# Kernel optimization log

Measured on AMD Instinct MI355X. Metric: run time of the kernel, lower is better.

## Reference

```python
import jax, jax.numpy as jnp
from jax import lax
import numpy as np

# dims
VOCAB = 64
B, L = 64, 2048
EMB = 128
D_MODEL = 128
N_LAYERS = 4
D_INNER = 256      # expand=2
D_STATE = 16
D_CONV = 4
DT_RANK = 8        # ceil(d_model/16)
NCLS = 3
BN_EPS = 1e-5
RMS_EPS = 1e-5


def setup_inputs():
    key = jax.random.key(0)
    ks = iter(jax.random.split(key, 48))
    def rn(shape, s=0.02):
        return jax.random.normal(next(ks), shape, jnp.float32) * s
    tokens = jax.random.randint(next(ks), (B, L), 0, VOCAB)
    mask = jnp.ones((B, L), jnp.float32)
    emb = rn((VOCAB, EMB)).at[0].set(0.0)  # padding_idx=0
    bn_w = jnp.ones((EMB,), jnp.float32)
    bn_b = jnp.zeros((EMB,), jnp.float32)
    conv_w = rn((D_MODEL, EMB, 3))
    conv_b = jnp.zeros((D_MODEL,), jnp.float32)
    in_proj_w = rn((N_LAYERS, 2 * D_INNER, D_MODEL))
    conv1d_w = rn((N_LAYERS, D_INNER, D_CONV), 0.1)
    conv1d_b = jnp.zeros((N_LAYERS, D_INNER), jnp.float32)
    x_proj_w = rn((N_LAYERS, DT_RANK + 2 * D_STATE, D_INNER))
    dt_proj_w = rn((N_LAYERS, D_INNER, DT_RANK), 0.1)
    dt_proj_b = rn((N_LAYERS, D_INNER), 0.1)
    A_log = jnp.tile(jnp.log(jnp.arange(1, D_STATE + 1, dtype=jnp.float32))[None, None, :],
                     (N_LAYERS, D_INNER, 1))
    D_param = jnp.ones((N_LAYERS, D_INNER), jnp.float32)
    out_proj_w = rn((N_LAYERS, D_MODEL, D_INNER))
    norm_w = jnp.ones((N_LAYERS, D_MODEL), jnp.float32)
    lin1_w = rn((512, D_MODEL)); lin1_b = jnp.zeros((512,), jnp.float32)
    lin2_w = rn((512, 512));     lin2_b = jnp.zeros((512,), jnp.float32)
    lin3_w = rn((NCLS, 512));    lin3_b = jnp.zeros((NCLS,), jnp.float32)
    return dict(tokens=tokens, mask=mask, emb=emb, bn_w=bn_w, bn_b=bn_b,
                conv_w=conv_w, conv_b=conv_b, in_proj_w=in_proj_w,
                conv1d_w=conv1d_w, conv1d_b=conv1d_b, x_proj_w=x_proj_w,
                dt_proj_w=dt_proj_w, dt_proj_b=dt_proj_b, A_log=A_log,
                D_param=D_param, out_proj_w=out_proj_w, norm_w=norm_w,
                lin1_w=lin1_w, lin1_b=lin1_b, lin2_w=lin2_w, lin2_b=lin2_b,
                lin3_w=lin3_w, lin3_b=lin3_b)


def _rmsnorm(x, w):
    return x * lax.rsqrt(jnp.mean(x * x, axis=-1, keepdims=True) + RMS_EPS) * w


def _selective_scan(u, dt, A, Bm, Cm, Dv):
    # u, dt: (B,L,di); A: (di,ds); Bm, Cm: (B,L,ds); Dv: (di,)
    def step(h, inp):
        dt_t, B_t, C_t, u_t = inp           # (B,di),(B,ds),(B,ds),(B,di)
        dA = jnp.exp(dt_t[:, :, None] * A)  # (B,di,ds)
        h = dA * h + (dt_t * u_t)[:, :, None] * B_t[:, None, :]
        y = jnp.einsum('bds,bs->bd', h, C_t)
        return h, y
    h0 = jnp.zeros((u.shape[0], A.shape[0], A.shape[1]), u.dtype)
    xs = (jnp.swapaxes(dt, 0, 1), jnp.swapaxes(Bm, 0, 1),
          jnp.swapaxes(Cm, 0, 1), jnp.swapaxes(u, 0, 1))
    _, ys = lax.scan(step, h0, xs)          # ys: (L,B,di)
    return jnp.swapaxes(ys, 0, 1) + u * Dv


def _mamba(x, in_w, cw, cb, xp_w, dtp_w, dtp_b, A_log, Dv, out_w):
    # x: (B,L,d_model)
    xz = jnp.einsum('bld,ed->ble', x, in_w)            # (B,L,2*di)
    xi, z = jnp.split(xz, 2, axis=-1)
    # causal depthwise conv over time
    xc = jnp.swapaxes(xi, 1, 2)                        # (B,di,L)
    xc = lax.conv_general_dilated(xc, cw[:, None, :], (1,), [(D_CONV - 1, 0)],
                                  dimension_numbers=('NCH', 'OIH', 'NCH'),
                                  feature_group_count=D_INNER)
    xc = jax.nn.silu(xc + cb[None, :, None])
    xc = jnp.swapaxes(xc, 1, 2)                        # (B,L,di)
    x_dbl = jnp.einsum('bld,ed->ble', xc, xp_w)        # (B,L,dtr+2*ds)
    dt = jax.nn.softplus(jnp.einsum('blr,dr->bld', x_dbl[..., :DT_RANK], dtp_w) + dtp_b)
    Bm = x_dbl[..., DT_RANK:DT_RANK + D_STATE]
    Cm = x_dbl[..., DT_RANK + D_STATE:]
    A = -jnp.exp(A_log)                                # (di,ds)
    y = _selective_scan(xc, dt, A, Bm, Cm, Dv)
    y = y * jax.nn.silu(z)
    return jnp.einsum('ble,de->bld', y, out_w)         # (B,L,d_model)


def _forward(tokens, mask, emb, bn_w, bn_b, conv_w, conv_b, in_proj_w,
             conv1d_w, conv1d_b, x_proj_w, dt_proj_w, dt_proj_b, A_log,
             D_param, out_proj_w, norm_w, lin1_w, lin1_b, lin2_w, lin2_b,
             lin3_w, lin3_b):
    x = emb[tokens]                                    # (B,L,E)
    xc = jnp.swapaxes(x, 1, 2)                         # (B,E,L)
    # BatchNorm1d in eval mode: running_mean=0, running_var=1
    xc = xc * (bn_w * lax.rsqrt(jnp.array(1.0 + BN_EPS)))[None, :, None] + bn_b[None, :, None]
    xc = lax.conv_general_dilated(xc, conv_w, (1,), [(1, 1)],
                                  dimension_numbers=('NCH', 'OIH', 'NCH'))
    xc = jax.nn.relu(xc + conv_b[None, :, None])
    x = jnp.swapaxes(xc, 1, 2)                         # (B,L,D_MODEL)
    for i in range(N_LAYERS):
        x = _mamba(_rmsnorm(x, norm_w[i]), in_proj_w[i], conv1d_w[i],
                   conv1d_b[i], x_proj_w[i], dt_proj_w[i], dt_proj_b[i],
                   A_log[i], D_param[i], out_proj_w[i]) + x
    # masked average pooling
    m = mask[:, :, None]
    denom = jnp.clip(jnp.sum(m, axis=1), 1e-9, None)   # (B,1)->(B,D) broadcast
    pooled = jnp.sum(x * m, axis=1) / denom
    h = jax.nn.relu(pooled @ lin1_w.T + lin1_b)
    h = jax.nn.relu(h @ lin2_w.T + lin2_b)
    return h @ lin3_w.T + lin3_b                       # (B,NCLS)


def reference(tokens, mask, emb, bn_w, bn_b, conv_w, conv_b, in_proj_w,
              conv1d_w, conv1d_b, x_proj_w, dt_proj_w, dt_proj_b, A_log,
              D_param, out_proj_w, norm_w, lin1_w, lin1_b, lin2_w, lin2_b,
              lin3_w, lin3_b):
    return _forward(tokens, mask, emb, bn_w, bn_b, conv_w, conv_b, in_proj_w,
                    conv1d_w, conv1d_b, x_proj_w, dt_proj_w, dt_proj_b, A_log,
                    D_param, out_proj_w, norm_w, lin1_w, lin1_b, lin2_w,
                    lin2_b, lin3_w, lin3_b)
```

## Files before the change

kernel.cpp:

```cpp
#include <hip/hip_runtime.h>
#include <math.h>

#define NB     64
#define SL     2048
#define NTOK   (NB*SL)
#define EMB_D  128
#define DMODEL 128
#define DIN    256
#define DST    16
#define NLAYER 4
#define SEG    64
#define NSEG   (SL/SEG)
#define L2E    1.4426950408889634f
#define LN2    0.6931471805599453f

typedef __bf16 bf16x8 __attribute__((ext_vector_type(8)));
typedef __bf16 bf16x4 __attribute__((ext_vector_type(4)));
typedef float  f32x4  __attribute__((ext_vector_type(4)));
typedef float  f32x2  __attribute__((ext_vector_type(2)));

#define FIX_PL   ((size_t)0)
#define FIX_PM   (FIX_PL + 131072)
#define FIX_PD   (FIX_PM + 1024)
#define FIX_H1   (FIX_PD + 8192)
#define FIX_H2   (FIX_H1 + 32768)
#define FIX_WP   (FIX_H2 + 32768)
#define FIX_W2B  (FIX_WP + 65536)
#define FIX_WINB (FIX_W2B + 24576)
#define FIX_WOUTB (FIX_WINB + 131072)
#define FIX_END  (FIX_WOUTB + 65536)

__device__ __forceinline__ float fexp2(float x){ return __builtin_amdgcn_exp2f(x); }
__device__ __forceinline__ float flog2(float x){ return __builtin_amdgcn_logf(x); }
__device__ __forceinline__ float frcp (float x){ return __builtin_amdgcn_rcpf(x); }
__device__ __forceinline__ float fast_exp(float x){ return fexp2(x*L2E); }
__device__ __forceinline__ float siluf(float v){ return v * frcp(1.f + fast_exp(-v)); }
__device__ __forceinline__ float softplusf(float a){
  return fmaxf(a,0.f) + flog2(1.f + fexp2(-fabsf(a)*L2E)) * LN2;
}
__device__ __forceinline__ unsigned short bfbits(float x){
  __bf16 b = (__bf16)x; return __builtin_bit_cast(unsigned short, b);
}
__device__ __forceinline__ unsigned int packdu(float dt, float u){
  return ((unsigned int)bfbits(u) << 16) | (unsigned int)bfbits(dt);
}

__device__ __forceinline__ f32x2 pkfma(f32x2 a, f32x2 b, f32x2 c){
#if __has_builtin(__builtin_elementwise_fma)
  return __builtin_elementwise_fma(a, b, c);
#else
  return (f32x2){ fmaf(a.x,b.x,c.x), fmaf(a.y,b.y,c.y) };
#endif
}

__global__ void k_w2b(const float* __restrict__ cw, __bf16* __restrict__ w2){
  int g = blockIdx.x*256 + threadIdx.x;
  if (g >= 128*384) return;
  int d = g / 384, j = g % 384;
  int k = j >> 7, e = j & 127;
  w2[d*384 + k*128 + e] = (__bf16)cw[d*384 + e*3 + k];
}

__global__ void k_cvt(const float* __restrict__ src, __bf16* __restrict__ dst, int n){
  int i = blockIdx.x*256 + threadIdx.x;
  if (i < n) dst[i] = (__bf16)src[i];
}

__global__ void k_wprep(const float* __restrict__ xpw, __bf16* __restrict__ wp){
  int g = blockIdx.x*256 + threadIdx.x;
  int l = g >> 14, rem = g & 16383;
  int n = rem >> 8, k = rem & 255;
  float v = (n < 40) ? xpw[(size_t)l*40*256 + n*256 + k] : 0.f;
  wp[g] = (__bf16)v;
}

__global__ void k_embed(const int* __restrict__ tok, const float* __restrict__ emb,
                        const float* __restrict__ bnw, const float* __restrict__ bnb,
                        float* __restrict__ xp){
  int r = blockIdx.x;
  int e = threadIdx.x;
  int b = r / 2050, tp = r % 2050;
  float v = 0.f;
  if (tp != 0 && tp != 2049){
    int t = tp - 1;
    int id = tok[(size_t)b*SL + t];
    float s = bnw[e] * rsqrtf(1.0f + 1e-5f);
    v = emb[(size_t)id*EMB_D + e] * s + bnb[e];
  }
  xp[(size_t)r*EMB_D + e] = v;
}

__global__ __launch_bounds__(256) void k_rmsscale(const float* __restrict__ x,
                                                  float* __restrict__ rs){
  int wv = threadIdx.x>>6, lane = threadIdx.x&63;
  size_t tok = (size_t)blockIdx.x*4 + wv;
  float2 v = *(const float2*)(x + tok*128 + lane*2);
  float ss = v.x*v.x + v.y*v.y;
  #pragma unroll
  for (int m=1;m<64;m<<=1) ss += __shfl_xor(ss, m);
  float r = rsqrtf(ss*(1.f/128.f) + 1e-5f);
  if (lane == 0) rs[tok] = r;
}

template<int MODE, int K, int N>
__global__ __launch_bounds__(256) void k_mgemm(
    const void* __restrict__ Av, const __bf16* __restrict__ Wb,
    const float* __restrict__ bias, const float* __restrict__ rsp,
    const float* __restrict__ nwp,
    float* __restrict__ out, __bf16* __restrict__ outb, __bf16* __restrict__ outz){
  __shared__ __bf16 As[128][40];
  __shared__ __bf16 Bs[128][40];
  const int tid  = threadIdx.x;
  const int wave = tid >> 6;
  const int lane = tid & 63;
  const int col  = lane & 15;
  const int quad = lane >> 4;
  const int wm = (wave & 1) * 64;
  const int wn = (wave >> 1) * 64;
  const int m0 = blockIdx.y * 128;
  const int n0 = blockIdx.x * 128;

  f32x4 acc[4][4];
  #pragma unroll
  for (int i=0;i<4;i++)
    #pragma unroll
    for (int j=0;j<4;j++) acc[i][j] = (f32x4){0.f,0.f,0.f,0.f};

  size_t abase;
  if constexpr(MODE==0){
    int bb = m0 >> 11, tloc = m0 & 2047;
    abase = ((size_t)bb*2050 + tloc) * 128;
  } else {
    abase = (size_t)m0 * K;
  }

  const int sm = tid >> 3;
  const int sk4 = (tid & 7) * 4;
  const int bn = tid >> 2;
  const int bk8 = (tid & 3) * 8;

  for (int k0 = 0; k0 < K; k0 += 32){
    #pragma unroll
    for (int p=0;p<4;p++){
      int m = p*32 + sm;
      const float* A = (const float*)Av;
      float4 v;
      if constexpr(MODE==0){
        v = *(const float4*)(A + abase + (size_t)m*128 + k0 + sk4);
      } else {
        float4 x4 = *(const float4*)(A + abase + (size_t)m*K + k0 + sk4);
        float4 w4 = *(const float4*)(nwp + k0 + sk4);
        float s = rsp[m0 + m];
        v.x = x4.x*s*w4.x; v.y = x4.y*s*w4.y; v.z = x4.z*s*w4.z; v.w = x4.w*s*w4.w;
      }
      bf16x4 o;
      o[0] = (__bf16)v.x; o[1] = (__bf16)v.y; o[2] = (__bf16)v.z; o[3] = (__bf16)v.w;
      *(bf16x4*)&As[m][sk4] = o;
    }
    #pragma unroll
    for (int p=0;p<2;p++){
      int n = p*64 + bn;
      bf16x8 w = *(const bf16x8*)(Wb + (size_t)(n0+n)*K + k0 + bk8);
      *(bf16x8*)&Bs[n][bk8] = w;
    }
    __syncthreads();
    bf16x8 af[4], bfr[4];
    const int fq = quad*8;
    #pragma unroll
    for (int i=0;i<4;i++) af[i]  = *(const bf16x8*)&As[wm + i*16 + col][fq];
    #pragma unroll
    for (int j=0;j<4;j++) bfr[j] = *(const bf16x8*)&Bs[wn + j*16 + col][fq];
    #pragma unroll
    for (int i=0;i<4;i++)
      #pragma unroll
      for (int j=0;j<4;j++)
        acc[i][j] = __builtin_amdgcn_mfma_f32_16x16x32_bf16(af[i], bfr[j], acc[i][j], 0, 0, 0);
    __syncthreads();
  }

  #pragma unroll
  for (int i=0;i<4;i++){
    #pragma unroll
    for (int j=0;j<4;j++){
      int n_l = wn + j*16 + col;
      #pragma unroll
      for (int r=0;r<4;r++){
        int m = m0 + wm + i*16 + quad*4 + r;
        float c = acc[i][j][r];
        if constexpr(MODE==0){
          int n = n0 + n_l;
          out[(size_t)m*DMODEL + n] = fmaxf(c + bias[n], 0.f);
        } else {
          int n = n0 + n_l;
          if (n < DIN) outb[(size_t)m*DIN + n]        = (__bf16)c;
          else         outz[(size_t)m*DIN + n - DIN]  = (__bf16)siluf(c);
        }
      }
    }
  }
}

__global__ __launch_bounds__(256) void k_seg(const __bf16* __restrict__ xi,
    const __bf16* __restrict__ wpb,
    const float* __restrict__ cw, const float* __restrict__ cb,
    const float* __restrict__ dtw, const float* __restrict__ dtb,
    const float* __restrict__ alog,
    float* __restrict__ vbc, unsigned int* __restrict__ dub,
    float* __restrict__ cseg, float* __restrict__ sdtb){
  __shared__ __bf16 sxc[64][264];
  __shared__ float vls[64][68];
  const int tid = threadIdx.x;
  const size_t m0 = (size_t)blockIdx.x * 64;
  const int b = (int)(m0 >> 11);
  const int g = (int)((m0 >> 6) & (NSEG-1));
  const int seq0 = (int)(m0 & 2047);

  {
    const int c4 = (tid & 63) * 4;
    const int tw = tid >> 6;
    float wc[4][4];
    #pragma unroll
    for (int j=0;j<4;j++)
      #pragma unroll
      for (int k=0;k<4;k++) wc[j][k] = cw[(c4+j)*4 + k];
    float4 cb4 = *(const float4*)(cb + c4);
    #pragma unroll
    for (int it=0; it<16; it++){
      int t = it*4 + tw;
      float4 acc = cb4;
      #pragma unroll
      for (int k=0;k<4;k++){
        if (seq0 + t - 3 + k >= 0){
          bf16x4 xv = *(const bf16x4*)(xi + (m0 + t - 3 + k)*DIN + c4);
          acc.x = fmaf(wc[0][k], (float)xv[0], acc.x);
          acc.y = fmaf(wc[1][k], (float)xv[1], acc.y);
          acc.z = fmaf(wc[2][k], (float)xv[2], acc.z);
          acc.w = fmaf(wc[3][k], (float)xv[3], acc.w);
        }
      }
      bf16x4 o;
      o[0]=(__bf16)siluf(acc.x); o[1]=(__bf16)siluf(acc.y);
      o[2]=(__bf16)siluf(acc.z); o[3]=(__bf16)siluf(acc.w);
      *(bf16x4*)&sxc[t][c4] = o;
    }
  }
  __syncthreads();

  {
    const int wave = tid >> 6, lane = tid & 63;
    const int col = lane & 15, quad = lane >> 4;
    const int wn = wave * 16;
    f32x4 acc[4];
    #pragma unroll
    for (int i=0;i<4;i++) acc[i] = (f32x4){0.f,0.f,0.f,0.f};
    #pragma unroll
    for (int kc=0;kc<8;kc++){
      bf16x8 bfr = *(const bf16x8*)(wpb + (size_t)(wn+col)*256 + kc*32 + quad*8);
      #pragma unroll
      for (int mi=0;mi<4;mi++){
        bf16x8 af = *(const bf16x8*)&sxc[mi*16 + col][kc*32 + quad*8];
        acc[mi] = __builtin_amdgcn_mfma_f32_16x16x32_bf16(af, bfr, acc[mi], 0, 0, 0);
      }
    }
    #pragma unroll
    for (int mi=0;mi<4;mi++)
      #pragma unroll
      for (int r=0;r<4;r++)
        vls[mi*16 + quad*4 + r][wn + col] = acc[mi][r];
  }
  __syncthreads();

  #pragma unroll
  for (int p=0;p<8;p++){
    int j = p*256 + tid;
    int t = j >> 5, i = j & 31;
    vbc[(m0+t)*32 + i] = vls[t][8+i];
  }

  {
    const int d = tid;
    const float a0 = -fast_exp(alog[d*DST]) * L2E;
    bool fast = true;
    for (int s=1;s<16;s++){
      float as = -fast_exp(alog[d*DST + s]) * L2E;
      fast = fast && (fabsf(as - (float)(s+1)*a0) <= 1e-3f*fabsf(as));
    }
    float4 w8a = *(const float4*)(dtw + d*8);
    float4 w8b = *(const float4*)(dtw + d*8 + 4);
    const f32x2 wA0 = {w8a.x, w8a.y}, wA1 = {w8a.z, w8a.w};
    const f32x2 wB0 = {w8b.x, w8b.y}, wB1 = {w8b.z, w8b.w};
    const float bd = dtb[d];
    float ssum = 0.f;
    size_t base = (((size_t)b*NSEG + g)*DIN + d)*DST;
    if (fast){
      f32x2 hp[8];
      #pragma unroll
      for (int k=0;k<8;k++) hp[k] = (f32x2){0.f,0.f};
      for (int t=0;t<SEG;t++){
        float4 v0 = *(const float4*)&vls[t][0];
        float4 v1 = *(const float4*)&vls[t][4];
        f32x2 la = pkfma((f32x2){v0.x,v0.y}, wA0, (f32x2){bd, 0.f});
        la = pkfma((f32x2){v0.z,v0.w}, wA1, la);
        la = pkfma((f32x2){v1.x,v1.y}, wB0, la);
        la = pkfma((f32x2){v1.z,v1.w}, wB1, la);
        float dt = softplusf(la.x + la.y);
        ssum += dt;
        float u = (float)sxc[t][d];
        dub[(m0+t)*DIN + d] = packdu(dt, u);
        float du = dt*u;
        float r1 = fexp2(dt*a0);
        float r2 = r1*r1, r4 = r2*r2, r8 = r4*r4;
        f32x2 p01 = {r1, r2};
        f32x2 s2 = {r2, r2}, s4 = {r4, r4}, s8 = {r8, r8};
        f32x2 p23 = p01*s2, p45 = p01*s4, p67 = p23*s4;
        f32x2 p89 = p01*s8, pAB = p23*s8, pCD = p45*s8, pEF = p67*s8;
        float4 b0 = *(const float4*)&vls[t][8];
        float4 b1 = *(const float4*)&vls[t][12];
        float4 b2 = *(const float4*)&vls[t][16];
        float4 b3 = *(const float4*)&vls[t][20];
        f32x2 du2 = {du, du};
        hp[0] = pkfma(p01, hp[0], du2*(f32x2){b0.x,b0.y});
        hp[1] = pkfma(p23, hp[1], du2*(f32x2){b0.z,b0.w});
        hp[2] = pkfma(p45, hp[2], du2*(f32x2){b1.x,b1.y});
        hp[3] = pkfma(p67, hp[3], du2*(f32x2){b1.z,b1.w});
        hp[4] = pkfma(p89, hp[4], du2*(f32x2){b2.x,b2.y});
        hp[5] = pkfma(pAB, hp[5], du2*(f32x2){b2.z,b2.w});
        hp[6] = pkfma(pCD, hp[6], du2*(f32x2){b3.x,b3.y});
        hp[7] = pkfma(pEF, hp[7], du2*(f32x2){b3.z,b3.w});
      }
      #pragma unroll
      for (int k=0;k<4;k++){
        float4 o = { hp[2*k].x, hp[2*k].y, hp[2*k+1].x, hp[2*k+1].y };
        *(float4*)(cseg + base + 4*k) = o;
      }
    } else {
      float h[16];
      float aA[16];
      #pragma unroll
      for (int k=0;k<16;k++){ h[k] = 0.f; aA[k] = -fast_exp(alog[d*DST + k]) * L2E; }
      for (int t=0;t<SEG;t++){
        float4 v0 = *(const float4*)&vls[t][0];
        float4 v1 = *(const float4*)&vls[t][4];
        float lin = bd;
        lin = fmaf(v0.x,w8a.x, fmaf(v0.y,w8a.y, fmaf(v0.z,w8a.z, fmaf(v0.w,w8a.w, lin))));
        lin = fmaf(v1.x,w8b.x, fmaf(v1.y,w8b.y, fmaf(v1.z,w8b.z, fmaf(v1.w,w8b.w, lin))));
        float dt = softplusf(lin);
        ssum += dt;
        float u = (float)sxc[t][d];
        dub[(m0+t)*DIN + d] = packdu(dt, u);
        float du = dt*u;
        #pragma unroll
        for (int k=0;k<16;k++){
          float e = fexp2(dt*aA[k]);
          h[k] = fmaf(e, h[k], du*vls[t][8+k]);
        }
      }
      #pragma unroll
      for (int k=0;k<4;k++){
        float4 o = { h[4*k], h[4*k+1], h[4*k+2], h[4*k+3] };
        *(float4*)(cseg + base + 4*k) = o;
      }
    }
    sdtb[((size_t)b*NSEG + g)*DIN + d] = ssum;
  }
}

__global__ __launch_bounds__(256) void k_scanB(float* __restrict__ cseg,
    const float* __restrict__ sdtb, const float* __restrict__ alog){
  int gl = blockIdx.x*256 + threadIdx.x;
  int b   = gl >> 12;
  int rem = gl & 4095;
  int d = rem >> 4, s = rem & 15;
  const float a = -fast_exp(alog[d*DST + s]) * L2E;
  float h = 0.f;
  for (int g=0; g<NSEG; g++){
    size_t base = ((size_t)b*NSEG + g)*DIN;
    float sd = sdtb[base + d];
    size_t ci = (base + d)*DST + s;
    float c = cseg[ci];
    cseg[ci] = h;
    h = fmaf(fexp2(a*sd), h, c);
  }
}

__global__ __launch_bounds__(256) void k_scanC3(float* __restrict__ xres,
    const unsigned int* __restrict__ dub, const float* __restrict__ vbc,
    const __bf16* __restrict__ gzb,
    const float* __restrict__ alog, const float* __restrict__ Dpar,
    const float* __restrict__ cseg, const __bf16* __restrict__ wout,
    float* __restrict__ rs){
  __shared__ __bf16 sy[64][264];
  __shared__ float svbc[64][32];
  float* sx = (float*)sy;
  const int tid = threadIdx.x;
  const size_t m0 = (size_t)blockIdx.x * 64;
  const int b = (int)(m0 >> 11);
  const int g = (int)((m0 >> 6) & (NSEG-1));

  #pragma unroll
  for (int p=0;p<8;p++){
    int j = p*256 + tid;
    int t = j >> 5, i = j & 31;
    svbc[t][i] = vbc[(m0+t)*32 + i];
  }

  {
    const int d = tid;
    const float a0 = -fast_exp(alog[d*DST]) * L2E;
    bool fast = true;
    for (int s=1;s<16;s++){
      float as = -fast_exp(alog[d*DST + s]) * L2E;
      fast = fast && (fabsf(as - (float)(s+1)*a0) <= 1e-3f*fabsf(as));
    }
    const float Dv = Dpar[d];
    size_t base = (((size_t)b*NSEG + g)*DIN + d)*DST;
    float4 hv0 = *(const float4*)(cseg + base);
    float4 hv1 = *(const float4*)(cseg + base + 4);
    float4 hv2 = *(const float4*)(cseg + base + 8);
    float4 hv3 = *(const float4*)(cseg + base + 12);
    __syncthreads();

    if (fast){
      f32x2 hp[8] = { {hv0.x,hv0.y},{hv0.z,hv0.w},{hv1.x,hv1.y},{hv1.z,hv1.w},
                      {hv2.x,hv2.y},{hv2.z,hv2.w},{hv3.x,hv3.y},{hv3.z,hv3.w} };

#define LOADCH(WV,GV,T0) \
      _Pragma("unroll") \
      for (int q=0;q<8;q++){ \
        WV[q] = dub[(m0 + (T0) + q)*DIN + d]; \
        GV[q] = gzb[(m0 + (T0) + q)*DIN + d]; \
      }

#define SCSTEP(T,WW,GG) { \
      float u  = __builtin_bit_cast(float, (WW) & 0xffff0000u); \
      float dt = __builtin_bit_cast(float, (WW) << 16); \
      float du = dt*u; \
      float r1 = fexp2(dt*a0); \
      float r2 = r1*r1, r4 = r2*r2, r8 = r4*r4; \
      f32x2 p01 = {r1, r2}; \
      f32x2 s2 = {r2, r2}, s4 = {r4, r4}, s8 = {r8, r8}; \
      f32x2 p23 = p01*s2, p45 = p01*s4, p67 = p23*s4; \
      f32x2 p89 = p01*s8, pAB = p23*s8, pCD = p45*s8, pEF = p67*s8; \
      float4 b0 = *(const float4*)&svbc[T][0]; \
      float4 b1 = *(const float4*)&svbc[T][4]; \
      float4 b2 = *(const float4*)&svbc[T][8]; \
      float4 b3 = *(const float4*)&svbc[T][12]; \
      float4 c0 = *(const float4*)&svbc[T][16]; \
      float4 c1 = *(const float4*)&svbc[T][20]; \
      float4 c2 = *(const float4*)&svbc[T][24]; \
      float4 c3 = *(const float4*)&svbc[T][28]; \
      f32x2 du2 = {du, du}; \
      f32x2 ya = {0.f,0.f}, yb = {0.f,0.f}; \
      hp[0] = pkfma(p01, hp[0], du2*(f32x2){b0.x,b0.y}); \
      ya = pkfma(hp[0], (f32x2){c0.x,c0.y}, ya); \
      hp[1] = pkfma(p23, hp[1], du2*(f32x2){b0.z,b0.w}); \
      yb = pkfma(hp[1], (f32x2){c0.z,c0.w}, yb); \
      hp[2] = pkfma(p45, hp[2], du2*(f32x2){b1.x,b1.y}); \
      ya = pkfma(hp[2], (f32x2){c1.x,c1.y}, ya); \
      hp[3] = pkfma(p67, hp[3], du2*(f32x2){b1.z,b1.w}); \
      yb = pkfma(hp[3], (f32x2){c1.z,c1.w}, yb); \
      hp[4] = pkfma(p89, hp[4], du2*(f32x2){b2.x,b2.y}); \
      ya = pkfma(hp[4], (f32x2){c2.x,c2.y}, ya); \
      hp[5] = pkfma(pAB, hp[5], du2*(f32x2){b2.z,b2.w}); \
      yb = pkfma(hp[5], (f32x2){c2.z,c2.w}, yb); \
      hp[6] = pkfma(pCD, hp[6], du2*(f32x2){b3.x,b3.y}); \
      ya = pkfma(hp[6], (f32x2){c3.x,c3.y}, ya); \
      hp[7] = pkfma(pEF, hp[7], du2*(f32x2){b3.z,b3.w}); \
      yb = pkfma(hp[7], (f32x2){c3.z,c3.w}, yb); \
      f32x2 ys = ya + yb; \
      float y = ys.x + ys.y; \
      sy[T][d] = (__bf16)((y + u*Dv) * (float)(GG)); }

      unsigned int wv0[8], wv1[8];
      __bf16 gv0[8], gv1[8];
      LOADCH(wv0, gv0, 0)
      #pragma unroll
      for (int tc=0; tc<SEG; tc+=16){
        LOADCH(wv1, gv1, tc+8)
        #pragma unroll
        for (int q=0;q<8;q++){ SCSTEP(tc+q, wv0[q], gv0[q]) }
        if (tc+16 < SEG){ LOADCH(wv0, gv0, tc+16) }
        #pragma unroll
        for (int q=0;q<8;q++){ SCSTEP(tc+8+q, wv1[q], gv1[q]) }
      }
#undef LOADCH
#undef SCSTEP
    } else {
      float h[16] = {hv0.x,hv0.y,hv0.z,hv0.w, hv1.x,hv1.y,hv1.z,hv1.w,
                     hv2.x,hv2.y,hv2.z,hv2.w, hv3.x,hv3.y,hv3.z,hv3.w};
      float aA[16];
      #pragma unroll
      for (int k=0;k<16;k++) aA[k] = -fast_exp(alog[d*DST + k]) * L2E;
      for (int t=0;t<SEG;t++){
        unsigned int w = dub[(m0+t)*DIN + d];
        float u  = __builtin_bit_cast(float, w & 0xffff0000u);
        float dt = __builtin_bit_cast(float, w << 16);
        float du = dt*u;
        float y = 0.f;
        #pragma unroll
        for (int k=0;k<16;k++){
          float e = fexp2(dt*aA[k]);
          h[k] = fmaf(e, h[k], du*svbc[t][k]);
          y = fmaf(h[k], svbc[t][16+k], y);
        }
        float gz = (float)gzb[(m0+t)*DIN + d];
        sy[t][d] = (__bf16)((y + u*Dv) * gz);
      }
    }
  }
  __syncthreads();

  const int wave = tid >> 6, lane = tid & 63;
  const int col = lane & 15, quad = lane >> 4;
  const int wn = wave * 32;
  f32x4 acc[4][2];
  #pragma unroll
  for (int i=0;i<4;i++)
    #pragma unroll
    for (int j=0;j<2;j++) acc[i][j] = (f32x4){0.f,0.f,0.f,0.f};
  #pragma unroll
  for (int kc=0;kc<8;kc++){
    bf16x8 bfr0 = *(const bf16x8*)(wout + (size_t)(wn +      col)*256 + kc*32 + quad*8);
    bf16x8 bfr1 = *(const bf16x8*)(wout + (size_t)(wn + 16 + col)*256 + kc*32 + quad*8);
    #pragma unroll
    for (int mi=0;mi<4;mi++){
      bf16x8 af = *(const bf16x8*)&sy[mi*16 + col][kc*32 + quad*8];
      acc[mi][0] = __builtin_amdgcn_mfma_f32_16x16x32_bf16(af, bfr0, acc[mi][0], 0, 0, 0);
      acc[mi][1] = __builtin_amdgcn_mfma_f32_16x16x32_bf16(af, bfr1, acc[mi][1], 0, 0, 0);
    }
  }
  __syncthreads();

  #pragma unroll
  for (int mi=0;mi<4;mi++){
    #pragma unroll
    for (int j=0;j<2;j++){
      int n = wn + j*16 + col;
      #pragma unroll
      for (int r=0;r<4;r++){
        int ml = mi*16 + quad*4 + r;
        size_t go = (m0 + ml)*DMODEL + n;
        float nx = xres[go] + acc[mi][j][r];
        xres[go] = nx;
        sx[ml*132 + n] = nx;
      }
    }
  }
  __syncthreads();
  {
    int row = tid >> 2, q = tid & 3;
    const float* pr = sx + row*132 + q*32;
    float ss = 0.f;
    #pragma unroll
    for (int i=0;i<32;i+=4){
      float4 v = *(const float4*)(pr + i);
      ss += v.x*v.x + v.y*v.y + v.z*v.z + v.w*v.w;
    }
    ss += __shfl_xor(ss, 1);
    ss += __shfl_xor(ss, 2);
    if (q == 0) rs[m0 + row] = rsqrtf(ss*(1.f/128.f) + 1e-5f);
  }
}

__global__ __launch_bounds__(256) void k_pool1(const float* __restrict__ x,
    const float* __restrict__ mask, float* __restrict__ part, float* __restrict__ pmask){
  int b = blockIdx.y, seg = blockIdx.x;
  int d = threadIdx.x & 127, half = threadIdx.x >> 7;
  int t0 = seg*128 + half*64;
  float acc = 0.f, macc = 0.f;
  for (int i=0;i<64;i++){
    int t = t0 + i;
    float mv = mask[(size_t)b*SL + t];
    acc = fmaf(x[((size_t)b*SL + t)*DMODEL + d], mv, acc);
    macc += mv;
  }
  __shared__ float sm[256];
  __shared__ float smm[2];
  sm[threadIdx.x] = acc;
  if (d == 0) smm[half] = macc;
  __syncthreads();
  if (half == 0){
    part[((size_t)b*16 + seg)*128 + d] = sm[d] + sm[128+d];
    if (d == 0) pmask[b*16 + seg] = smm[0] + smm[1];
  }
}

__global__ void k_pool2(const float* __restrict__ part, const float* __restrict__ pmask,
                        float* __restrict__ pooled){
  int b = blockIdx.x, d = threadIdx.x;
  float acc = 0.f, ms = 0.f;
  for (int s=0;s<16;s++){ acc += part[((size_t)b*16+s)*128 + d]; ms += pmask[b*16+s]; }
  pooled[(size_t)b*128 + d] = acc / fmaxf(ms, 1e-9f);
}

__global__ void k_mlp_a(const float* __restrict__ in, const float* __restrict__ w,
                        const float* __restrict__ bias, float* __restrict__ out, int K){
  int b = blockIdx.y;
  int n = blockIdx.x*128 + threadIdx.x;
  const float4* pw = (const float4*)(w + (size_t)n*K);
  const float4* pi = (const float4*)(in + (size_t)b*K);
  float acc = 0.f;
  for (int k=0;k<K/4;k++){
    float4 a = pi[k], ww = pw[k];
    acc = fmaf(a.x,ww.x, fmaf(a.y,ww.y, fmaf(a.z,ww.z, fmaf(a.w,ww.w, acc))));
  }
  out[(size_t)b*512 + n] = fmaxf(acc + bias[n], 0.f);
}

__global__ void k_mlp3(const float* __restrict__ h, const float* __restrict__ w,
                       const float* __restrict__ bias, float* __restrict__ out){
  int b = blockIdx.x;
  int n = threadIdx.x >> 6, lane = threadIdx.x & 63;
  if (n >= 3) return;
  float acc = 0.f;
  for (int k=lane; k<512; k+=64) acc = fmaf(h[(size_t)b*512+k], w[(size_t)n*512+k], acc);
  #pragma unroll
  for (int m=1;m<64;m<<=1) acc += __shfl_xor(acc, m);
  if (lane == 0) out[(size_t)b*3 + n] = acc + bias[n];
}

extern "C" void kernel_launch(void* const* d_in, const int* in_sizes, int n_in,
                              void* d_out, int out_size, void* d_ws, size_t ws_size,
                              hipStream_t stream){
  const int*   tokens = (const int*)  d_in[0];
  const float* mask   = (const float*)d_in[1];
  const float* emb    = (const float*)d_in[2];
  const float* bn_w   = (const float*)d_in[3];
  const float* bn_b   = (const float*)d_in[4];
  const float* conv_w = (const float*)d_in[5];
  const float* conv_b = (const float*)d_in[6];
  const float* in_w   = (const float*)d_in[7];
  const float* c1_w   = (const float*)d_in[8];
  const float* c1_b   = (const float*)d_in[9];
  const float* xp_w   = (const float*)d_in[10];
  const float* dtp_w  = (const float*)d_in[11];
  const float* dtp_b  = (const float*)d_in[12];
  const float* A_log  = (const float*)d_in[13];
  const float* D_par  = (const float*)d_in[14];
  const float* out_w  = (const float*)d_in[15];
  const float* nrm_w  = (const float*)d_in[16];
  const float* l1w = (const float*)d_in[17]; const float* l1b = (const float*)d_in[18];
  const float* l2w = (const float*)d_in[19]; const float* l2b = (const float*)d_in[20];
  const float* l3w = (const float*)d_in[21]; const float* l3b = (const float*)d_in[22];
  float* dout = (float*)d_out;

  int CB = 64;
  while (CB > 1 && ((size_t)CB*SL*741 + FIX_END)*4 > ws_size) CB >>= 1;
  if (((size_t)CB*SL*741 + FIX_END)*4 > ws_size) return;
  const size_t CTOK = (size_t)CB*SL;

  float* ws  = (float*)d_ws;
  float* pl  = ws + FIX_PL;
  float* pm  = ws + FIX_PM;
  float* pd  = ws + FIX_PD;
  float* h1  = ws + FIX_H1;
  float* h2  = ws + FIX_H2;
  __bf16* wpb   = (__bf16*)(ws + FIX_WP);
  __bf16* w2b   = (__bf16*)(ws + FIX_W2B);
  __bf16* winb  = (__bf16*)(ws + FIX_WINB);
  __bf16* woutb = (__bf16*)(ws + FIX_WOUTB);
  float* xcb = ws + FIX_END;
  float* rs  = xcb + CTOK*128;
  __bf16* xib = (__bf16*)(rs + CTOK);
  unsigned int* dub = (unsigned int*)(xib + CTOK*256);
  float* pad = (float*)xib;
  float* vbc = (float*)(dub + CTOK*256);
  float* csg = vbc + CTOK*32;
  float* sdt = csg + CTOK*64;
  __bf16* zb  = (__bf16*)(sdt + CTOK*4);

  k_w2b<<<192, 256, 0, stream>>>(conv_w, w2b);
  k_cvt<<<1024, 256, 0, stream>>>(in_w,  winb,  4*512*128);
  k_cvt<<<512,  256, 0, stream>>>(out_w, woutb, 4*128*256);
  k_wprep<<<256, 256, 0, stream>>>(xp_w, wpb);

  const int nchunks = NB / CB;
  for (int c = 0; c < nchunks; c++){
    const int* tok_c = tokens + (size_t)c*CTOK;

    k_embed<<<CB*2050, 128, 0, stream>>>(tok_c, emb, bn_w, bn_b, pad);
    k_mgemm<0,384,128><<<dim3(1, CTOK/128), 256, 0, stream>>>(
        pad, w2b, conv_b, nullptr, nullptr, xcb, nullptr, nullptr);
    k_rmsscale<<<CTOK/4, 256, 0, stream>>>(xcb, rs);

    for (int layer = 0; layer < NLAYER; layer++){
      const __bf16* lin = winb  + (size_t)layer*512*128;
      const float* lcw  = c1_w  + (size_t)layer*DIN*4;
      const float* lcb  = c1_b  + (size_t)layer*DIN;
      const float* ldw  = dtp_w + (size_t)layer*DIN*8;
      const float* ldb  = dtp_b + (size_t)layer*DIN;
      const float* lal  = A_log + (size_t)layer*DIN*DST;
      const float* lD   = D_par + (size_t)layer*DIN;
      const __bf16* low = woutb + (size_t)layer*128*256;
      const float* lnw  = nrm_w + (size_t)layer*128;

      k_mgemm<1,128,512><<<dim3(4, CTOK/128), 256, 0, stream>>>(
          xcb, lin, nullptr, rs, lnw, nullptr, xib, zb);
      k_seg<<<(int)(CTOK/64), 256, 0, stream>>>(
          xib, wpb + (size_t)layer*64*256, lcw, lcb, ldw, ldb, lal, vbc, dub, csg, sdt);
      k_scanB<<<CB*16, 256, 0, stream>>>(csg, sdt, lal);
      k_scanC3<<<(int)(CTOK/64), 256, 0, stream>>>(
          xcb, dub, vbc, zb, lal, lD, csg, low, rs);
    }

    k_pool1<<<dim3(16, CB), 256, 0, stream>>>(
        xcb, mask + (size_t)c*CTOK, pl + (size_t)c*CB*16*128, pm + (size_t)c*CB*16);
  }

  k_pool2<<<NB, 128, 0, stream>>>(pl, pm, pd);
  k_mlp_a<<<dim3(4, NB), 128, 0, stream>>>(pd, l1w, l1b, h1, 128);
  k_mlp_a<<<dim3(4, NB), 128, 0, stream>>>(h1, l2w, l2b, h2, 512);
  k_mlp3<<<NB, 256, 0, stream>>>(h2, l3w, l3b, dout);
}
```

Before: 1.389 ms.

## Fuse embedding into conv GEMM, fuse MLP head, prefetch scan operands

Embedding lookup and batchnorm scaling now happen inside the first GEMM's A-tile load, so the padded embedding buffer is never written and read back. The pooling and three MLP layers become one kernel per batch row. The depthwise conv in k_seg keeps a sliding register window instead of reloading four rows per output. The k_seg and scanC loops load next-step LDS operands one iteration ahead, and scanB loads all segment values before its serial recurrence. These changes remove launches and memory traffic and hide latency, at the cost of more registers, which can lower occupancy.

```diff
diff --git a/kernel.cpp b/kernel.cpp
--- a/kernel.cpp
+++ b/kernel.cpp
@@ -74,22 +74,6 @@
   wp[g] = (__bf16)v;
 }
 
-__global__ void k_embed(const int* __restrict__ tok, const float* __restrict__ emb,
-                        const float* __restrict__ bnw, const float* __restrict__ bnb,
-                        float* __restrict__ xp){
-  int r = blockIdx.x;
-  int e = threadIdx.x;
-  int b = r / 2050, tp = r % 2050;
-  float v = 0.f;
-  if (tp != 0 && tp != 2049){
-    int t = tp - 1;
-    int id = tok[(size_t)b*SL + t];
-    float s = bnw[e] * rsqrtf(1.0f + 1e-5f);
-    v = emb[(size_t)id*EMB_D + e] * s + bnb[e];
-  }
-  xp[(size_t)r*EMB_D + e] = v;
-}
-
 __global__ __launch_bounds__(256) void k_rmsscale(const float* __restrict__ x,
                                                   float* __restrict__ rs){
   int wv = threadIdx.x>>6, lane = threadIdx.x&63;
@@ -106,7 +90,7 @@
 __global__ __launch_bounds__(256) void k_mgemm(
     const void* __restrict__ Av, const __bf16* __restrict__ Wb,
     const float* __restrict__ bias, const float* __restrict__ rsp,
-    const float* __restrict__ nwp,
+    const float* __restrict__ nwp, const float* __restrict__ bnbp,
     float* __restrict__ out, __bf16* __restrict__ outb, __bf16* __restrict__ outz){
   __shared__ __bf16 As[128][40];
   __shared__ __bf16 Bs[128][40];
@@ -126,36 +110,54 @@
     #pragma unroll
     for (int j=0;j<4;j++) acc[i][j] = (f32x4){0.f,0.f,0.f,0.f};
 
-  size_t abase;
-  if constexpr(MODE==0){
-    int bb = m0 >> 11, tloc = m0 & 2047;
-    abase = ((size_t)bb*2050 + tloc) * 128;
-  } else {
-    abase = (size_t)m0 * K;
-  }
-
   const int sm = tid >> 3;
   const int sk4 = (tid & 7) * 4;
   const int bn = tid >> 2;
   const int bk8 = (tid & 3) * 8;
 
   for (int k0 = 0; k0 < K; k0 += 32){
-    #pragma unroll
-    for (int p=0;p<4;p++){
-      int m = p*32 + sm;
-      const float* A = (const float*)Av;
-      float4 v;
-      if constexpr(MODE==0){
-        v = *(const float4*)(A + abase + (size_t)m*128 + k0 + sk4);
-      } else {
+    if constexpr(MODE==0){
+      const int* tok = (const int*)Av;
+      const int tap = k0 >> 7;
+      const int e = (k0 & 127) + sk4;
+      const float sc = rsqrtf(1.0f + 1e-5f);
+      float4 bw4 = *(const float4*)(nwp + e);
+      float4 bb4 = *(const float4*)(bnbp + e);
+      float4 s4;
+      s4.x = bw4.x*sc; s4.y = bw4.y*sc; s4.z = bw4.z*sc; s4.w = bw4.w*sc;
+      #pragma unroll
+      for (int p=0;p<4;p++){
+        int m = p*32 + sm;
+        int tokpos = m0 + m;
+        int t = (tokpos & 2047) + tap - 1;
+        float4 v = {0.f,0.f,0.f,0.f};
+        if ((unsigned)t < 2048u){
+          int id = tok[((size_t)(tokpos >> 11) << 11) + t];
+          float4 ev = *(const float4*)(rsp + (size_t)id*EMB_D + e);
+          v.x = fmaf(ev.x, s4.x, bb4.x);
+          v.y = fmaf(ev.y, s4.y, bb4.y);
+          v.z = fmaf(ev.z, s4.z, bb4.z);
+          v.w = fmaf(ev.w, s4.w, bb4.w);
+        }
+        bf16x4 o;
+        o[0] = (__bf16)v.x; o[1] = (__bf16)v.y; o[2] = (__bf16)v.z; o[3] = (__bf16)v.w;
+        *(bf16x4*)&As[m][sk4] = o;
+      }
+    } else {
+      const size_t abase = (size_t)m0 * K;
+      #pragma unroll
+      for (int p=0;p<4;p++){
+        int m = p*32 + sm;
+        const float* A = (const float*)Av;
         float4 x4 = *(const float4*)(A + abase + (size_t)m*K + k0 + sk4);
         float4 w4 = *(const float4*)(nwp + k0 + sk4);
         float s = rsp[m0 + m];
+        float4 v;
         v.x = x4.x*s*w4.x; v.y = x4.y*s*w4.y; v.z = x4.z*s*w4.z; v.w = x4.w*s*w4.w;
-      }
-      bf16x4 o;
-      o[0] = (__bf16)v.x; o[1] = (__bf16)v.y; o[2] = (__bf16)v.z; o[3] = (__bf16)v.w;
-      *(bf16x4*)&As[m][sk4] = o;
+        bf16x4 o;
+        o[0] = (__bf16)v.x; o[1] = (__bf16)v.y; o[2] = (__bf16)v.z; o[3] = (__bf16)v.w;
+        *(bf16x4*)&As[m][sk4] = o;
+      }
     }
     #pragma unroll
     for (int p=0;p<2;p++){
@@ -218,30 +220,42 @@
   {
     const int c4 = (tid & 63) * 4;
     const int tw = tid >> 6;
+    const int t0 = tw * 16;
     float wc[4][4];
     #pragma unroll
     for (int j=0;j<4;j++)
       #pragma unroll
       for (int k=0;k<4;k++) wc[j][k] = cw[(c4+j)*4 + k];
     float4 cb4 = *(const float4*)(cb + c4);
-    #pragma unroll
-    for (int it=0; it<16; it++){
-      int t = it*4 + tw;
+    bf16x4 zed;
+    zed[0] = (__bf16)0.f; zed[1] = (__bf16)0.f; zed[2] = (__bf16)0.f; zed[3] = (__bf16)0.f;
+    bf16x4 win[3];
+    #pragma unroll
+    for (int j=0;j<3;j++){
+      int tr = t0 - 3 + j;
+      win[j] = (seq0 + tr >= 0) ? *(const bf16x4*)(xi + (m0 + tr)*DIN + c4) : zed;
+    }
+    #pragma unroll
+    for (int i=0;i<16;i++){
+      int t = t0 + i;
+      bf16x4 w3 = *(const bf16x4*)(xi + (m0 + t)*DIN + c4);
       float4 acc = cb4;
       #pragma unroll
-      for (int k=0;k<4;k++){
-        if (seq0 + t - 3 + k >= 0){
-          bf16x4 xv = *(const bf16x4*)(xi + (m0 + t - 3 + k)*DIN + c4);
-          acc.x = fmaf(wc[0][k], (float)xv[0], acc.x);
-          acc.y = fmaf(wc[1][k], (float)xv[1], acc.y);
-          acc.z = fmaf(wc[2][k], (float)xv[2], acc.z);
-          acc.w = fmaf(wc[3][k], (float)xv[3], acc.w);
-        }
-      }
+      for (int k=0;k<3;k++){
+        acc.x = fmaf(wc[0][k], (float)win[k][0], acc.x);
+        acc.y = fmaf(wc[1][k], (float)win[k][1], acc.y);
+        acc.z = fmaf(wc[2][k], (float)win[k][2], acc.z);
+        acc.w = fmaf(wc[3][k], (float)win[k][3], acc.w);
+      }
+      acc.x = fmaf(wc[0][3], (float)w3[0], acc.x);
+      acc.y = fmaf(wc[1][3], (float)w3[1], acc.y);
+      acc.z = fmaf(wc[2][3], (float)w3[2], acc.z);
+      acc.w = fmaf(wc[3][3], (float)w3[3], acc.w);
       bf16x4 o;
       o[0]=(__bf16)siluf(acc.x); o[1]=(__bf16)siluf(acc.y);
       o[2]=(__bf16)siluf(acc.z); o[3]=(__bf16)siluf(acc.w);
       *(bf16x4*)&sxc[t][c4] = o;
+      win[0] = win[1]; win[1] = win[2]; win[2] = w3;
     }
   }
   __syncthreads();
@@ -296,16 +310,31 @@
       f32x2 hp[8];
       #pragma unroll
       for (int k=0;k<8;k++) hp[k] = (f32x2){0.f,0.f};
+      float4 cv0 = *(const float4*)&vls[0][0];
+      float4 cv1 = *(const float4*)&vls[0][4];
+      float4 cb0 = *(const float4*)&vls[0][8];
+      float4 cb1 = *(const float4*)&vls[0][12];
+      float4 cb2 = *(const float4*)&vls[0][16];
+      float4 cb3 = *(const float4*)&vls[0][20];
+      float cu = (float)sxc[0][d];
+      #pragma unroll 2
       for (int t=0;t<SEG;t++){
-        float4 v0 = *(const float4*)&vls[t][0];
-        float4 v1 = *(const float4*)&vls[t][4];
+        float4 v0=cv0, v1=cv1, b0=cb0, b1=cb1, b2=cb2, b3=cb3;
+        float u = cu;
+        int tn = (t < SEG-1) ? t+1 : SEG-1;
+        cv0 = *(const float4*)&vls[tn][0];
+        cv1 = *(const float4*)&vls[tn][4];
+        cb0 = *(const float4*)&vls[tn][8];
+        cb1 = *(const float4*)&vls[tn][12];
+        cb2 = *(const float4*)&vls[tn][16];
+        cb3 = *(const float4*)&vls[tn][20];
+        cu = (float)sxc[tn][d];
         f32x2 la = pkfma((f32x2){v0.x,v0.y}, wA0, (f32x2){bd, 0.f});
         la = pkfma((f32x2){v0.z,v0.w}, wA1, la);
         la = pkfma((f32x2){v1.x,v1.y}, wB0, la);
         la = pkfma((f32x2){v1.z,v1.w}, wB1, la);
         float dt = softplusf(la.x + la.y);
         ssum += dt;
-        float u = (float)sxc[t][d];
         dub[(m0+t)*DIN + d] = packdu(dt, u);
         float du = dt*u;
         float r1 = fexp2(dt*a0);
@@ -314,10 +343,6 @@
         f32x2 s2 = {r2, r2}, s4 = {r4, r4}, s8 = {r8, r8};
         f32x2 p23 = p01*s2, p45 = p01*s4, p67 = p23*s4;
         f32x2 p89 = p01*s8, pAB = p23*s8, pCD = p45*s8, pEF = p67*s8;
-        float4 b0 = *(const float4*)&vls[t][8];
-        float4 b1 = *(const float4*)&vls[t][12];
-        float4 b2 = *(const float4*)&vls[t][16];
-        float4 b3 = *(const float4*)&vls[t][20];
         f32x2 du2 = {du, du};
         hp[0] = pkfma(p01, hp[0], du2*(f32x2){b0.x,b0.y});
         hp[1] = pkfma(p23, hp[1], du2*(f32x2){b0.z,b0.w});
@@ -372,14 +397,20 @@
   int rem = gl & 4095;
   int d = rem >> 4, s = rem & 15;
   const float a = -fast_exp(alog[d*DST + s]) * L2E;
-  float h = 0.f;
+  float cvals[NSEG];
+  float sdv[NSEG];
+  #pragma unroll
   for (int g=0; g<NSEG; g++){
     size_t base = ((size_t)b*NSEG + g)*DIN;
-    float sd = sdtb[base + d];
-    size_t ci = (base + d)*DST + s;
-    float c = cseg[ci];
+    sdv[g]   = sdtb[base + d];
+    cvals[g] = cseg[(base + d)*DST + s];
+  }
+  float h = 0.f;
+  #pragma unroll
+  for (int g=0; g<NSEG; g++){
+    size_t ci = (((size_t)b*NSEG + g)*DIN + d)*DST + s;
     cseg[ci] = h;
-    h = fmaf(fexp2(a*sd), h, c);
+    h = fmaf(fexp2(a*sdv[g]), h, cvals[g]);
   }
 }
 
@@ -432,6 +463,15 @@
       }
 
 #define SCSTEP(T,WW,GG) { \
+      int Tn = ((T) < SEG-1) ? (T)+1 : SEG-1; \
+      float4 nb0 = *(const float4*)&svbc[Tn][0]; \
+      float4 nb1 = *(const float4*)&svbc[Tn][4]; \
+      float4 nb2 = *(const float4*)&svbc[Tn][8]; \
+      float4 nb3 = *(const float4*)&svbc[Tn][12]; \
+      float4 nb4 = *(const float4*)&svbc[Tn][16]; \
+      float4 nb5 = *(const float4*)&svbc[Tn][20]; \
+      float4 nb6 = *(const float4*)&svbc[Tn][24]; \
+      float4 nb7 = *(const float4*)&svbc[Tn][28]; \
       float u  = __builtin_bit_cast(float, (WW) & 0xffff0000u); \
       float dt = __builtin_bit_cast(float, (WW) << 16); \
       float du = dt*u; \
@@ -441,39 +481,40 @@
       f32x2 s2 = {r2, r2}, s4 = {r4, r4}, s8 = {r8, r8}; \
       f32x2 p23 = p01*s2, p45 = p01*s4, p67 = p23*s4; \
       f32x2 p89 = p01*s8, pAB = p23*s8, pCD = p45*s8, pEF = p67*s8; \
-      float4 b0 = *(const float4*)&svbc[T][0]; \
-      float4 b1 = *(const float4*)&svbc[T][4]; \
-      float4 b2 = *(const float4*)&svbc[T][8]; \
-      float4 b3 = *(const float4*)&svbc[T][12]; \
-      float4 c0 = *(const float4*)&svbc[T][16]; \
-      float4 c1 = *(const float4*)&svbc[T][20]; \
-      float4 c2 = *(const float4*)&svbc[T][24]; \
-      float4 c3 = *(const float4*)&svbc[T][28]; \
       f32x2 du2 = {du, du}; \
       f32x2 ya = {0.f,0.f}, yb = {0.f,0.f}; \
-      hp[0] = pkfma(p01, hp[0], du2*(f32x2){b0.x,b0.y}); \
-      ya = pkfma(hp[0], (f32x2){c0.x,c0.y}, ya); \
-      hp[1] = pkfma(p23, hp[1], du2*(f32x2){b0.z,b0.w}); \
-      yb = pkfma(hp[1], (f32x2){c0.z,c0.w}, yb); \
-      hp[2] = pkfma(p45, hp[2], du2*(f32x2){b1.x,b1.y}); \
-      ya = pkfma(hp[2], (f32x2){c1.x,c1.y}, ya); \
-      hp[3] = pkfma(p67, hp[3], du2*(f32x2){b1.z,b1.w}); \
-      yb = pkfma(hp[3], (f32x2){c1.z,c1.w}, yb); \
-      hp[4] = pkfma(p89, hp[4], du2*(f32x2){b2.x,b2.y}); \
-      ya = pkfma(hp[4], (f32x2){c2.x,c2.y}, ya); \
-      hp[5] = pkfma(pAB, hp[5], du2*(f32x2){b2.z,b2.w}); \
-      yb = pkfma(hp[5], (f32x2){c2.z,c2.w}, yb); \
-      hp[6] = pkfma(pCD, hp[6], du2*(f32x2){b3.x,b3.y}); \
-      ya = pkfma(hp[6], (f32x2){c3.x,c3.y}, ya); \
-      hp[7] = pkfma(pEF, hp[7], du2*(f32x2){b3.z,b3.w}); \
-      yb = pkfma(hp[7], (f32x2){c3.z,c3.w}, yb); \
+      hp[0] = pkfma(p01, hp[0], du2*(f32x2){pb0.x,pb0.y}); \
+      ya = pkfma(hp[0], (f32x2){pb4.x,pb4.y}, ya); \
+      hp[1] = pkfma(p23, hp[1], du2*(f32x2){pb0.z,pb0.w}); \
+      yb = pkfma(hp[1], (f32x2){pb4.z,pb4.w}, yb); \
+      hp[2] = pkfma(p45, hp[2], du2*(f32x2){pb1.x,pb1.y}); \
+      ya = pkfma(hp[2], (f32x2){pb5.x,pb5.y}, ya); \
+      hp[3] = pkfma(p67, hp[3], du2*(f32x2){pb1.z,pb1.w}); \
+      yb = pkfma(hp[3], (f32x2){pb5.z,pb5.w}, yb); \
+      hp[4] = pkfma(p89, hp[4], du2*(f32x2){pb2.x,pb2.y}); \
+      ya = pkfma(hp[4], (f32x2){pb6.x,pb6.y}, ya); \
+      hp[5] = pkfma(pAB, hp[5], du2*(f32x2){pb2.z,pb2.w}); \
+      yb = pkfma(hp[5], (f32x2){pb6.z,pb6.w}, yb); \
+      hp[6] = pkfma(pCD, hp[6], du2*(f32x2){pb3.x,pb3.y}); \
+      ya = pkfma(hp[6], (f32x2){pb7.x,pb7.y}, ya); \
+      hp[7] = pkfma(pEF, hp[7], du2*(f32x2){pb3.z,pb3.w}); \
+      yb = pkfma(hp[7], (f32x2){pb7.z,pb7.w}, yb); \
       f32x2 ys = ya + yb; \
       float y = ys.x + ys.y; \
-      sy[T][d] = (__bf16)((y + u*Dv) * (float)(GG)); }
+      sy[T][d] = (__bf16)((y + u*Dv) * (float)(GG)); \
+      pb0=nb0; pb1=nb1; pb2=nb2; pb3=nb3; pb4=nb4; pb5=nb5; pb6=nb6; pb7=nb7; }
 
       unsigned int wv0[8], wv1[8];
       __bf16 gv0[8], gv1[8];
       LOADCH(wv0, gv0, 0)
+      float4 pb0 = *(const float4*)&svbc[0][0];
+      float4 pb1 = *(const float4*)&svbc[0][4];
+      float4 pb2 = *(const float4*)&svbc[0][8];
+      float4 pb3 = *(const float4*)&svbc[0][12];
+      float4 pb4 = *(const float4*)&svbc[0][16];
+      float4 pb5 = *(const float4*)&svbc[0][20];
+      float4 pb6 = *(const float4*)&svbc[0][24];
+      float4 pb7 = *(const float4*)&svbc[0][28];
       #pragma unroll
       for (int tc=0; tc<SEG; tc+=16){
         LOADCH(wv1, gv1, tc+8)
@@ -585,38 +626,60 @@
   }
 }
 
-__global__ void k_pool2(const float* __restrict__ part, const float* __restrict__ pmask,
-                        float* __restrict__ pooled){
-  int b = blockIdx.x, d = threadIdx.x;
-  float acc = 0.f, ms = 0.f;
-  for (int s=0;s<16;s++){ acc += part[((size_t)b*16+s)*128 + d]; ms += pmask[b*16+s]; }
-  pooled[(size_t)b*128 + d] = acc / fmaxf(ms, 1e-9f);
-}
-
-__global__ void k_mlp_a(const float* __restrict__ in, const float* __restrict__ w,
-                        const float* __restrict__ bias, float* __restrict__ out, int K){
-  int b = blockIdx.y;
-  int n = blockIdx.x*128 + threadIdx.x;
-  const float4* pw = (const float4*)(w + (size_t)n*K);
-  const float4* pi = (const float4*)(in + (size_t)b*K);
-  float acc = 0.f;
-  for (int k=0;k<K/4;k++){
-    float4 a = pi[k], ww = pw[k];
-    acc = fmaf(a.x,ww.x, fmaf(a.y,ww.y, fmaf(a.z,ww.z, fmaf(a.w,ww.w, acc))));
-  }
-  out[(size_t)b*512 + n] = fmaxf(acc + bias[n], 0.f);
-}
-
-__global__ void k_mlp3(const float* __restrict__ h, const float* __restrict__ w,
-                       const float* __restrict__ bias, float* __restrict__ out){
-  int b = blockIdx.x;
-  int n = threadIdx.x >> 6, lane = threadIdx.x & 63;
-  if (n >= 3) return;
-  float acc = 0.f;
-  for (int k=lane; k<512; k+=64) acc = fmaf(h[(size_t)b*512+k], w[(size_t)n*512+k], acc);
-  #pragma unroll
-  for (int m=1;m<64;m<<=1) acc += __shfl_xor(acc, m);
-  if (lane == 0) out[(size_t)b*3 + n] = acc + bias[n];
+__global__ __launch_bounds__(512) void k_head(const float* __restrict__ part,
+    const float* __restrict__ pmask,
+    const float* __restrict__ l1w, const float* __restrict__ l1b,
+    const float* __restrict__ l2w, const float* __restrict__ l2b,
+    const float* __restrict__ l3w, const float* __restrict__ l3b,
+    float* __restrict__ out){
+  __shared__ float sp[128];
+  __shared__ float sh[512];
+  int b = blockIdx.x, tid = threadIdx.x;
+  if (tid < 128){
+    float acc = 0.f, ms = 0.f;
+    for (int s=0;s<16;s++){
+      acc += part[((size_t)b*16+s)*128 + tid];
+      ms  += pmask[b*16+s];
+    }
+    sp[tid] = acc / fmaxf(ms, 1e-9f);
+  }
+  __syncthreads();
+  {
+    const float4* pw = (const float4*)(l1w + (size_t)tid*128);
+    const float4* pi = (const float4*)sp;
+    float acc = 0.f;
+    #pragma unroll 8
+    for (int k=0;k<32;k++){
+      float4 a = pi[k], w = pw[k];
+      acc = fmaf(a.x,w.x, fmaf(a.y,w.y, fmaf(a.z,w.z, fmaf(a.w,w.w, acc))));
+    }
+    __syncthreads();
+    sh[tid] = fmaxf(acc + l1b[tid], 0.f);
+  }
+  __syncthreads();
+  float h2v;
+  {
+    const float4* pw = (const float4*)(l2w + (size_t)tid*512);
+    const float4* pi = (const float4*)sh;
+    float acc = 0.f;
+    #pragma unroll 8
+    for (int k=0;k<128;k++){
+      float4 a = pi[k], w = pw[k];
+      acc = fmaf(a.x,w.x, fmaf(a.y,w.y, fmaf(a.z,w.z, fmaf(a.w,w.w, acc))));
+    }
+    h2v = fmaxf(acc + l2b[tid], 0.f);
+  }
+  __syncthreads();
+  sh[tid] = h2v;
+  __syncthreads();
+  if (tid < 192){
+    int n = tid >> 6, lane = tid & 63;
+    float acc = 0.f;
+    for (int k=lane; k<512; k+=64) acc = fmaf(sh[k], l3w[(size_t)n*512+k], acc);
+    #pragma unroll
+    for (int m=1;m<64;m<<=1) acc += __shfl_xor(acc, m);
+    if (lane == 0) out[(size_t)b*3 + n] = acc + l3b[n];
+  }
 }
 
 extern "C" void kernel_launch(void* const* d_in, const int* in_sizes, int n_in,
@@ -652,9 +715,6 @@
   float* ws  = (float*)d_ws;
   float* pl  = ws + FIX_PL;
   float* pm  = ws + FIX_PM;
-  float* pd  = ws + FIX_PD;
-  float* h1  = ws + FIX_H1;
-  float* h2  = ws + FIX_H2;
   __bf16* wpb   = (__bf16*)(ws + FIX_WP);
   __bf16* w2b   = (__bf16*)(ws + FIX_W2B);
   __bf16* winb  = (__bf16*)(ws + FIX_WINB);
@@ -663,7 +723,6 @@
   float* rs  = xcb + CTOK*128;
   __bf16* xib = (__bf16*)(rs + CTOK);
   unsigned int* dub = (unsigned int*)(xib + CTOK*256);
-  float* pad = (float*)xib;
   float* vbc = (float*)(dub + CTOK*256);
   float* csg = vbc + CTOK*32;
   float* sdt = csg + CTOK*64;
@@ -678,9 +737,8 @@
   for (int c = 0; c < nchunks; c++){
     const int* tok_c = tokens + (size_t)c*CTOK;
 
-    k_embed<<<CB*2050, 128, 0, stream>>>(tok_c, emb, bn_w, bn_b, pad);
     k_mgemm<0,384,128><<<dim3(1, CTOK/128), 256, 0, stream>>>(
-        pad, w2b, conv_b, nullptr, nullptr, xcb, nullptr, nullptr);
+        tok_c, w2b, conv_b, emb, bn_w, bn_b, xcb, nullptr, nullptr);
     k_rmsscale<<<CTOK/4, 256, 0, stream>>>(xcb, rs);
 
     for (int layer = 0; layer < NLAYER; layer++){
@@ -695,7 +753,7 @@
       const float* lnw  = nrm_w + (size_t)layer*128;
 
       k_mgemm<1,128,512><<<dim3(4, CTOK/128), 256, 0, stream>>>(
-          xcb, lin, nullptr, rs, lnw, nullptr, xib, zb);
+          xcb, lin, nullptr, rs, lnw, nullptr, nullptr, xib, zb);
       k_seg<<<(int)(CTOK/64), 256, 0, stream>>>(
           xib, wpb + (size_t)layer*64*256, lcw, lcb, ldw, ldb, lal, vbc, dub, csg, sdt);
       k_scanB<<<CB*16, 256, 0, stream>>>(csg, sdt, lal);
@@ -707,8 +765,5 @@
         xcb, mask + (size_t)c*CTOK, pl + (size_t)c*CB*16*128, pm + (size_t)c*CB*16);
   }
 
-  k_pool2<<<NB, 128, 0, stream>>>(pl, pm, pd);
-  k_mlp_a<<<dim3(4, NB), 128, 0, stream>>>(pd, l1w, l1b, h1, 128);
-  k_mlp_a<<<dim3(4, NB), 128, 0, stream>>>(h1, l2w, l2b, h2, 512);
-  k_mlp3<<<NB, 256, 0, stream>>>(h2, l3w, l3b, dout);
-}
+  k_head<<<NB, 512, 0, stream>>>(pl, pm, l1w, l1b, l2w, l2b, l3w, l3b, dout);
+}
```

New measurement: 1.348 ms. 2.9% less time.
